# Kernel tuning notes

Hardware: AMD Instinct MI355X
Metric: run time of the kernel (lower is better)

## Reference

```python
import jax, jax.numpy as jnp
import numpy as np

B, C, H, W, D = 2, 512, 16, 16, 16
GROUPS = 32
EPS = 1e-6


def setup_inputs() -> dict:
    key = jax.random.key(0)
    ks = jax.random.split(key, 6)
    s = 1.0 / np.sqrt(C)
    inp = {
        "x": jax.random.normal(ks[0], (B, C, H, W, D), jnp.float32),
        "gn_w": jnp.ones((C,), jnp.float32),
        "gn_b": jnp.zeros((C,), jnp.float32),
        "wq": jax.random.normal(ks[1], (C, C), jnp.float32) * s,
        "bq": jnp.zeros((C,), jnp.float32),
        "wk": jax.random.normal(ks[2], (C, C), jnp.float32) * s,
        "bk": jnp.zeros((C,), jnp.float32),
        "wv": jax.random.normal(ks[3], (C, C), jnp.float32) * s,
        "bv": jnp.zeros((C,), jnp.float32),
        "wp": jax.random.normal(ks[4], (C, C), jnp.float32) * s,
        "bp": jnp.zeros((C,), jnp.float32),
    }
    return inp


def reference(x, gn_w, gn_b, wq, bq, wk, bk, wv, bv, wp, bp):
    b, c, h, w, d = x.shape
    # GroupNorm(32 groups, eps=1e-6, affine)
    xg = x.reshape(b, GROUPS, c // GROUPS, h, w, d)
    mu = xg.mean(axis=(2, 3, 4, 5), keepdims=True)
    var = xg.var(axis=(2, 3, 4, 5), keepdims=True)
    hn = ((xg - mu) / jnp.sqrt(var + EPS)).reshape(b, c, h, w, d)
    hn = hn * gn_w[None, :, None, None, None] + gn_b[None, :, None, None, None]
    # 1x1x1 conv projections == per-token channel matmul
    n = h * w * d
    hf = hn.reshape(b, c, n)
    q = jnp.einsum('oc,bcn->bon', wq, hf) + bq[None, :, None]  # [b,c,n]
    k = jnp.einsum('oc,bcn->bon', wk, hf) + bk[None, :, None]
    v = jnp.einsum('oc,bcn->bon', wv, hf) + bv[None, :, None]
    # attention: scores[b,i,j] = sum_c q[b,c,i] k[b,c,j] / sqrt(c)
    scores = jnp.einsum('bci,bcj->bij', q, k) * (c ** -0.5)
    attn = jax.nn.softmax(scores, axis=2)  # [b,n,n]
    # out[b,c,i] = sum_j v[b,c,j] attn[b,i,j]
    o = jnp.einsum('bij,bcj->bci', attn, v)
    o = jnp.einsum('oc,bcn->bon', wp, o) + bp[None, :, None]
    return x + o.reshape(b, c, h, w, d)
```

## Files before the change

### kernel.cpp

```cpp
#include <hip/hip_runtime.h>
#include <hip/hip_bf16.h>
#include <stdint.h>

typedef short short8 __attribute__((ext_vector_type(8)));
typedef float f32x4  __attribute__((ext_vector_type(4)));
typedef float f32x2  __attribute__((ext_vector_type(2)));
typedef float f32x16 __attribute__((ext_vector_type(16)));
typedef int   i32x4  __attribute__((ext_vector_type(4)));
typedef int   i32x8  __attribute__((ext_vector_type(8)));
typedef unsigned char uchar;

#define B_ 2
#define C_ 512
#define N_ 4096
#define G_ 32
#define WN (C_ * C_)
#define PREP_BLOCKS 4101

static __device__ __forceinline__ short f2bf(float f) {
    return __builtin_bit_cast(short, __float2bfloat16(f));
}
static __device__ __forceinline__ uchar f2fp8(float f) {
    return (uchar)(__builtin_amdgcn_cvt_pk_fp8_f32(f, f, 0, false) & 0xff);
}

static __device__ __forceinline__ void async16(uchar* lds_wave_base, const uchar* g) {
    auto l  = (__attribute__((address_space(3))) unsigned int*)(uintptr_t)(lds_wave_base);
    auto gg = (const __attribute__((address_space(1))) unsigned int*)(g);
    __builtin_amdgcn_global_load_lds(gg, l, 16, 0, 0);
}

__global__ void prep_stats(const float* __restrict__ wq, const float* __restrict__ wk,
                           const float* __restrict__ wv, const float* __restrict__ wp,
                           const float* __restrict__ bq, const float* __restrict__ bk,
                           const float* __restrict__ x,
                           uchar* __restrict__ Wb, float* __restrict__ bqk,
                           float* __restrict__ raw) {
    if (blockIdx.x < PREP_BLOCKS) {
        int i = blockIdx.x * 256 + threadIdx.x;
        if (i < 4 * WN) {
            const float* src = (i < 2*WN) ? ((i < WN) ? wq : wk) : ((i < 3*WN) ? wv : wp);
            Wb[i] = f2fp8(src[i & (WN - 1)] * 16.f);
        } else if (i < 4*WN + 1024) {
            int j = i - 4*WN;
            bqk[j] = (j < C_) ? bq[j] : bk[j - C_];
        }
        return;
    }
    const int idx = blockIdx.x - PREP_BLOCKS;
    const int bg = idx >> 2, qt = idx & 3;
    const float4* p = (const float4*)(x + (size_t)bg * 16 * N_ + (size_t)qt * 4 * N_);
    int tid = threadIdx.x;
    float s = 0.f, sq = 0.f;
    #pragma unroll
    for (int rep = 0; rep < 16; rep++) {
        float4 t = p[rep * 256 + tid];
        s  += t.x + t.y + t.z + t.w;
        sq += t.x*t.x + t.y*t.y + t.z*t.z + t.w*t.w;
    }
    __shared__ float rs[256], rq[256];
    rs[tid] = s; rq[tid] = sq;
    __syncthreads();
    for (int h = 128; h > 0; h >>= 1) {
        if (tid < h) { rs[tid] += rs[tid+h]; rq[tid] += rq[tid+h]; }
        __syncthreads();
    }
    if (tid == 0) {
        raw[idx*2+0] = rs[0];
        raw[idx*2+1] = rq[0];
    }
}

__global__ void gn_apply(const float* __restrict__ x, const float* __restrict__ raw,
                         const float* __restrict__ gw, const float* __restrict__ gb,
                         uchar* __restrict__ hn) {
    __shared__ uchar t[64 * 68];
    const int n0 = blockIdx.x * 64, c0 = blockIdx.y * 64, b = blockIdx.z;
    const int lane = threadIdx.x & 63, w = threadIdx.x >> 6;
    const float inv = 1.f / (16.f * N_);
    #pragma unroll
    for (int rep = 0; rep < 16; rep++) {
        int c  = rep * 4 + w;
        int cc = c0 + c;
        int g  = cc >> 4;
        int base = (b*G_ + g) * 8;
        float mean = (raw[base] + raw[base+2] + raw[base+4] + raw[base+6]) * inv;
        float var  = (raw[base+1] + raw[base+3] + raw[base+5] + raw[base+7]) * inv - mean * mean;
        float rstd = rsqrtf(var + 1e-6f);
        float sc = gw[cc] * rstd;
        float bi = gb[cc] - mean * sc;
        float v = x[((size_t)(b*C_ + cc)) * N_ + n0 + lane];
        t[lane*68 + c] = f2fp8(v * sc + bi);
    }
    __syncthreads();
    #pragma unroll
    for (int rep = 0; rep < 16; rep++) {
        int n = rep * 4 + w;
        hn[((size_t)(b*N_ + n0 + n)) * C_ + c0 + lane] = t[n*68 + lane];
    }
}

template<int BM, int BIAS_MODE, int OUT_MODE, int K, int SWZ>
__global__ __launch_bounds__(256, 3)
void gemm_nt8(const uchar* __restrict__ A, int lda, long long sAz,
              const uchar* __restrict__ Bm, int ldb, long long sBz,
              void* __restrict__ Cv, int ldc, long long sCz,
              const float* __restrict__ bias,
              const float* __restrict__ res,
              float alpha) {
    constexpr int MI = BM / 64;
    constexpr int T  = K / 64;
    constexpr int D  = (BM == 128) ? 4 : 3;
    constexpr unsigned WAITD = 0xF70u | D;
    constexpr unsigned WAIT0 = 0xF70u;
    __shared__ uchar As[3][BM * 64];
    __shared__ uchar Bs[3][128 * 64];

    int bx, by, bz;
    if (SWZ == 1) {
        int fid = blockIdx.x;
        int xcd = fid & 7, j = fid >> 3;
        int gg = (j >> 2) * 8 + xcd;
        bx = j & 3; by = gg & 63; bz = gg >> 6;
    } else if (SWZ == 2) {
        int fid = blockIdx.x;
        int xcd = fid & 7, j = fid >> 3;
        bz = j >> 7;
        int r = j & 127;
        by = (xcd << 2) | (r >> 5);
        bx = r & 31;
    } else { bx = blockIdx.x; by = blockIdx.y; bz = blockIdx.z; }

    const int tid  = threadIdx.x;
    const int lane = tid & 63;
    const int wid  = tid >> 6;
    const int wr   = wid >> 1;
    const int wc   = wid & 1;
    const int m0 = by * BM;
    const int n0 = bx * 128;

    const int r  = tid >> 2;
    const int gc = (tid & 3) ^ ((r >> 1) & 3);
    const uchar* Ap  = A  + sAz * bz + (size_t)(m0 + r) * lda + gc * 16;
    const uchar* Ap1 = Ap + (size_t)64 * lda;
    const uchar* Bp  = Bm + sBz * bz + (size_t)(n0 + r) * ldb + gc * 16;
    const uchar* Bp1 = Bp + (size_t)64 * ldb;

    f32x16 acc[MI][2];
    #pragma unroll
    for (int i = 0; i < MI; i++)
        #pragma unroll
        for (int j = 0; j < 2; j++)
            #pragma unroll
            for (int e = 0; e < 16; e++)
                acc[i][j][e] = 0.f;

    const int rl = lane & 31;
    const int hk = (lane >> 5) * 2;

    #define ISSUE(IB, u) do { size_t _kb = (size_t)(u) * 64; \
        async16(&As[IB][wid * 1024], Ap + _kb); \
        if (BM == 128) async16(&As[IB][4096 + wid * 1024], Ap1 + _kb); \
        async16(&Bs[IB][wid * 1024], Bp + _kb); \
        async16(&Bs[IB][4096 + wid * 1024], Bp1 + _kb); } while (0)

    #define STEP(Bf, DO_ISSUE, IB, u, DO_BAR, WIMM) do { \
        i32x8 af[MI], bf[2]; \
        _Pragma("unroll") \
        for (int i = 0; i < MI; i++) { \
            int ar = wr*(BM/2) + i*32 + rl; \
            int ao = ar*64 + ((hk ^ ((ar>>1)&3)) << 4); \
            *(i32x4*)&af[i]       = *(const i32x4*)&As[Bf][ao]; \
            *(((i32x4*)&af[i])+1) = *(const i32x4*)&As[Bf][ao ^ 16]; \
        } \
        _Pragma("unroll") \
        for (int i = 0; i < 2; i++) { \
            int br = wc*64 + i*32 + rl; \
            int bo = br*64 + ((hk ^ ((br>>1)&3)) << 4); \
            *(i32x4*)&bf[i]       = *(const i32x4*)&Bs[Bf][bo]; \
            *(((i32x4*)&bf[i])+1) = *(const i32x4*)&Bs[Bf][bo ^ 16]; \
        } \
        if (DO_ISSUE) ISSUE(IB, u); \
        _Pragma("unroll") \
        for (int mi = 0; mi < MI; mi++) \
            _Pragma("unroll") \
            for (int ni = 0; ni < 2; ni++) \
                acc[mi][ni] = __builtin_amdgcn_mfma_scale_f32_32x32x64_f8f6f4( \
                    af[mi], bf[ni], acc[mi][ni], 0, 0, 0, 127, 0, 127); \
        if (DO_BAR) { __builtin_amdgcn_s_waitcnt(WIMM); __builtin_amdgcn_s_barrier(); } \
    } while (0)

    ISSUE(0, 0);
    ISSUE(1, 1);
    __builtin_amdgcn_s_waitcnt(WAITD);
    __builtin_amdgcn_s_barrier();

    constexpr int Gm = (T - 2) / 3;
    for (int m = 0; m < Gm; m++) {
        STEP(0, 1, 2, m*3 + 2, 1, WAITD);
        STEP(1, 1, 0, m*3 + 3, 1, WAITD);
        STEP(2, 1, 1, m*3 + 4, 1, WAITD);
    }
    if (T - 3*Gm == 2) {
        STEP(0, 0, 0, 0, 1, WAIT0);
        STEP(1, 0, 0, 0, 0, 0);
    } else {
        STEP(0, 1, 2, T-2, 1, WAITD);
        STEP(1, 1, 0, T-1, 1, WAITD);
        STEP(2, 0, 0, 0, 1, WAIT0);
        STEP(0, 0, 0, 0, 0, 0);
    }
    #undef ISSUE
    #undef STEP

    const int rh = (lane >> 5) * 4;
    #pragma unroll
    for (int mi = 0; mi < MI; mi++) {
        #pragma unroll
        for (int ni = 0; ni < 2; ni++) {
            int cc = n0 + wc*64 + ni*32 + rl;
            float cb = (BIAS_MODE == 1) ? bias[cc] : 0.f;
            #pragma unroll
            for (int g = 0; g < 4; g++) {
                #pragma unroll
                for (int r4 = 0; r4 < 4; r4++) {
                    int rr = m0 + wr*(BM/2) + mi*32 + g*8 + rh + r4;
                    float val = acc[mi][ni][g*4 + r4] * alpha + cb;
                    if (BIAS_MODE == 2) val += bias[rr];
                    long long idx = sCz * bz + (long long)rr * ldc + cc;
                    if (OUT_MODE == 0)      ((short*)Cv)[idx] = f2bf(val);
                    else if (OUT_MODE == 2) ((float*)Cv)[idx] = val + res[idx];
                    else                    ((uchar*)Cv)[idx] = f2fp8(val);
                }
            }
        }
    }
}

__global__ void softmax_rows8(uchar* __restrict__ S) {
    const int lane = threadIdx.x & 63;
    const int wave = threadIdx.x >> 6;
    const size_t row = (size_t)blockIdx.x * 4 + wave;
    uint4* rp = (uint4*)(S + row * N_);
    uint4 d[4];
    float f[64];
    float mx = -3.0e38f;
    #pragma unroll
    for (int c = 0; c < 4; c++) {
        d[c] = rp[c * 64 + lane];
        unsigned wv[4] = {d[c].x, d[c].y, d[c].z, d[c].w};
        #pragma unroll
        for (int u = 0; u < 4; u++) {
            f32x2 lo = __builtin_amdgcn_cvt_pk_f32_fp8(wv[u], false);
            f32x2 hi = __builtin_amdgcn_cvt_pk_f32_fp8(wv[u], true);
            int b = c*16 + u*4;
            f[b+0] = lo[0]; f[b+1] = lo[1]; f[b+2] = hi[0]; f[b+3] = hi[1];
            mx = fmaxf(mx, fmaxf(fmaxf(lo[0], lo[1]), fmaxf(hi[0], hi[1])));
        }
    }
    #pragma unroll
    for (int off = 32; off > 0; off >>= 1)
        mx = fmaxf(mx, __shfl_xor(mx, off));
    float sum = 0.f;
    const float k = 0.0625f;
    #pragma unroll
    for (int j = 0; j < 64; j++) { f[j] = __expf((f[j] - mx) * k); sum += f[j]; }
    #pragma unroll
    for (int off = 32; off > 0; off >>= 1)
        sum += __shfl_xor(sum, off);
    float inv = 256.f / sum;
    #pragma unroll
    for (int c = 0; c < 4; c++) {
        unsigned wv[4];
        #pragma unroll
        for (int u = 0; u < 4; u++) {
            int b = c*16 + u*4;
            int o = 0;
            o = __builtin_amdgcn_cvt_pk_fp8_f32(f[b+0]*inv, f[b+1]*inv, o, false);
            o = __builtin_amdgcn_cvt_pk_fp8_f32(f[b+2]*inv, f[b+3]*inv, o, true);
            wv[u] = (unsigned)o;
        }
        uint4 ov; ov.x = wv[0]; ov.y = wv[1]; ov.z = wv[2]; ov.w = wv[3];
        rp[c * 64 + lane] = ov;
    }
}

extern "C" void kernel_launch(void* const* d_in, const int* in_sizes, int n_in,
                              void* d_out, int out_size, void* d_ws, size_t ws_size,
                              hipStream_t stream) {
    const float* x   = (const float*)d_in[0];
    const float* gnw = (const float*)d_in[1];
    const float* gnb = (const float*)d_in[2];
    const float* wq  = (const float*)d_in[3];
    const float* bq  = (const float*)d_in[4];
    const float* wk  = (const float*)d_in[5];
    const float* bk  = (const float*)d_in[6];
    const float* wv  = (const float*)d_in[7];
    const float* bv  = (const float*)d_in[8];
    const float* wp  = (const float*)d_in[9];
    const float* bp  = (const float*)d_in[10];
    float* out = (float*)d_out;
    char*  ws  = (char*)d_ws;

    float* raw = (float*)(ws + 0);
    float* bqk = (float*)(ws + 8192);
    uchar* Wb  = (uchar*)(ws + 65536);
    uchar* Hn  = (uchar*)(ws + (2ull  << 20));
    uchar* QK8 = (uchar*)(ws + (8ull  << 20));
    uchar* V8  = (uchar*)(ws + (16ull << 20));
    uchar* Ot8 = (uchar*)(ws + (20ull << 20));
    uchar* Sb  = (uchar*)(ws + (24ull << 20));

    prep_stats<<<PREP_BLOCKS + 256, 256, 0, stream>>>(wq, wk, wv, wp, bq, bk, x, Wb, bqk, raw);
    gn_apply<<<dim3(N_/64, C_/64, B_), 256, 0, stream>>>(x, raw, gnw, gnb, Hn);

    const long long sHn = (long long)N_ * C_;
    const long long sQK = (long long)N_ * 1024;
    const long long sV  = (long long)C_ * N_;
    const long long sS  = (long long)N_ * N_;

    gemm_nt8<128,1,3,512,0><<<dim3(8, 32, 2), 256, 0, stream>>>(
        Hn, C_, sHn, Wb, C_, 0, QK8, 1024, sQK, bqk, nullptr, 1.f/16.f);
    gemm_nt8<64,2,3,512,0><<<dim3(32, 8, 2), 256, 0, stream>>>(
        Wb + 2*WN, C_, 0, Hn, C_, sHn, V8, N_, sV, bv, nullptr, 1.f/16.f);

    const float alphaS = 0.044194173824159216f * 16.f;
    gemm_nt8<128,0,3,512,2><<<2048, 256, 0, stream>>>(
        QK8, 1024, sQK, QK8 + 512, 1024, sQK, Sb, N_, sS, nullptr, nullptr, alphaS);
    softmax_rows8<<<B_*N_/4, 256, 0, stream>>>(Sb);
    gemm_nt8<64,0,3,4096,1><<<512, 256, 0, stream>>>(
        Sb, N_, sS, V8, N_, sV, Ot8, C_, sHn, nullptr, nullptr, 1.f/16.f);
    gemm_nt8<64,2,2,512,0><<<dim3(32, 8, 2), 256, 0, stream>>>(
        Wb + 3*WN, C_, 0, Ot8, C_, sHn, out, N_, (long long)C_*N_, bp, x, 1.f/256.f);
}
```

Before: 188.0 us.

## Replace LDS-staged triple-buffered GEMM with direct global-to-register fragment loads

The fp8 GEMM kernel no longer stages A and B tiles through triple-buffered LDS with async global_load_lds and barriers. Each wave now loads its MFMA fragments straight from global memory into registers, unrolled four k-steps at a time, and the launch-bounds occupancy hint drops from 3 to 2 blocks to make room for the larger register footprint. This removes LDS traffic and barrier synchronisation. In exchange, waves in the same block no longer share tile loads, so global and L2 traffic goes up, and the loop has no software overlap between loads and MFMAs beyond what the unrolling gives.

```diff
diff --git a/kernel.cpp b/kernel.cpp
--- a/kernel.cpp
+++ b/kernel.cpp
@@ -22,12 +22,6 @@
 }
 static __device__ __forceinline__ uchar f2fp8(float f) {
     return (uchar)(__builtin_amdgcn_cvt_pk_fp8_f32(f, f, 0, false) & 0xff);
-}
-
-static __device__ __forceinline__ void async16(uchar* lds_wave_base, const uchar* g) {
-    auto l  = (__attribute__((address_space(3))) unsigned int*)(uintptr_t)(lds_wave_base);
-    auto gg = (const __attribute__((address_space(1))) unsigned int*)(g);
-    __builtin_amdgcn_global_load_lds(gg, l, 16, 0, 0);
 }
 
 __global__ void prep_stats(const float* __restrict__ wq, const float* __restrict__ wk,
@@ -101,7 +95,7 @@
 }
 
 template<int BM, int BIAS_MODE, int OUT_MODE, int K, int SWZ>
-__global__ __launch_bounds__(256, 3)
+__global__ __launch_bounds__(256, 2)
 void gemm_nt8(const uchar* __restrict__ A, int lda, long long sAz,
               const uchar* __restrict__ Bm, int ldb, long long sBz,
               void* __restrict__ Cv, int ldc, long long sCz,
@@ -110,11 +104,6 @@
               float alpha) {
     constexpr int MI = BM / 64;
     constexpr int T  = K / 64;
-    constexpr int D  = (BM == 128) ? 4 : 3;
-    constexpr unsigned WAITD = 0xF70u | D;
-    constexpr unsigned WAIT0 = 0xF70u;
-    __shared__ uchar As[3][BM * 64];
-    __shared__ uchar Bs[3][128 * 64];
 
     int bx, by, bz;
     if (SWZ == 1) {
@@ -139,12 +128,17 @@
     const int m0 = by * BM;
     const int n0 = bx * 128;
 
-    const int r  = tid >> 2;
-    const int gc = (tid & 3) ^ ((r >> 1) & 3);
-    const uchar* Ap  = A  + sAz * bz + (size_t)(m0 + r) * lda + gc * 16;
-    const uchar* Ap1 = Ap + (size_t)64 * lda;
-    const uchar* Bp  = Bm + sBz * bz + (size_t)(n0 + r) * ldb + gc * 16;
-    const uchar* Bp1 = Bp + (size_t)64 * ldb;
+    const int rl = lane & 31;
+    const int kh = (lane >> 5) * 32;
+
+    const uchar* Ab[MI];
+    #pragma unroll
+    for (int i = 0; i < MI; i++)
+        Ab[i] = A + sAz * bz + (size_t)(m0 + wr*(BM/2) + i*32 + rl) * lda + kh;
+    const uchar* Bb[2];
+    #pragma unroll
+    for (int i = 0; i < 2; i++)
+        Bb[i] = Bm + sBz * bz + (size_t)(n0 + wc*64 + i*32 + rl) * ldb + kh;
 
     f32x16 acc[MI][2];
     #pragma unroll
@@ -155,63 +149,35 @@
             for (int e = 0; e < 16; e++)
                 acc[i][j][e] = 0.f;
 
-    const int rl = lane & 31;
-    const int hk = (lane >> 5) * 2;
-
-    #define ISSUE(IB, u) do { size_t _kb = (size_t)(u) * 64; \
-        async16(&As[IB][wid * 1024], Ap + _kb); \
-        if (BM == 128) async16(&As[IB][4096 + wid * 1024], Ap1 + _kb); \
-        async16(&Bs[IB][wid * 1024], Bp + _kb); \
-        async16(&Bs[IB][4096 + wid * 1024], Bp1 + _kb); } while (0)
-
-    #define STEP(Bf, DO_ISSUE, IB, u, DO_BAR, WIMM) do { \
-        i32x8 af[MI], bf[2]; \
-        _Pragma("unroll") \
-        for (int i = 0; i < MI; i++) { \
-            int ar = wr*(BM/2) + i*32 + rl; \
-            int ao = ar*64 + ((hk ^ ((ar>>1)&3)) << 4); \
-            *(i32x4*)&af[i]       = *(const i32x4*)&As[Bf][ao]; \
-            *(((i32x4*)&af[i])+1) = *(const i32x4*)&As[Bf][ao ^ 16]; \
-        } \
-        _Pragma("unroll") \
-        for (int i = 0; i < 2; i++) { \
-            int br = wc*64 + i*32 + rl; \
-            int bo = br*64 + ((hk ^ ((br>>1)&3)) << 4); \
-            *(i32x4*)&bf[i]       = *(const i32x4*)&Bs[Bf][bo]; \
-            *(((i32x4*)&bf[i])+1) = *(const i32x4*)&Bs[Bf][bo ^ 16]; \
-        } \
-        if (DO_ISSUE) ISSUE(IB, u); \
-        _Pragma("unroll") \
-        for (int mi = 0; mi < MI; mi++) \
-            _Pragma("unroll") \
-            for (int ni = 0; ni < 2; ni++) \
-                acc[mi][ni] = __builtin_amdgcn_mfma_scale_f32_32x32x64_f8f6f4( \
-                    af[mi], bf[ni], acc[mi][ni], 0, 0, 0, 127, 0, 127); \
-        if (DO_BAR) { __builtin_amdgcn_s_waitcnt(WIMM); __builtin_amdgcn_s_barrier(); } \
-    } while (0)
-
-    ISSUE(0, 0);
-    ISSUE(1, 1);
-    __builtin_amdgcn_s_waitcnt(WAITD);
-    __builtin_amdgcn_s_barrier();
-
-    constexpr int Gm = (T - 2) / 3;
-    for (int m = 0; m < Gm; m++) {
-        STEP(0, 1, 2, m*3 + 2, 1, WAITD);
-        STEP(1, 1, 0, m*3 + 3, 1, WAITD);
-        STEP(2, 1, 1, m*3 + 4, 1, WAITD);
-    }
-    if (T - 3*Gm == 2) {
-        STEP(0, 0, 0, 0, 1, WAIT0);
-        STEP(1, 0, 0, 0, 0, 0);
-    } else {
-        STEP(0, 1, 2, T-2, 1, WAITD);
-        STEP(1, 1, 0, T-1, 1, WAITD);
-        STEP(2, 0, 0, 0, 1, WAIT0);
-        STEP(0, 0, 0, 0, 0, 0);
-    }
-    #undef ISSUE
-    #undef STEP
+    for (int uo = 0; uo < T / 4; uo++) {
+        i32x8 af[4][MI], bf[4][2];
+        #pragma unroll
+        for (int ui = 0; ui < 4; ui++) {
+            int kb = ui * 64;
+            #pragma unroll
+            for (int i = 0; i < MI; i++) {
+                *(i32x4*)&af[ui][i]       = *(const i32x4*)(Ab[i] + kb);
+                *(((i32x4*)&af[ui][i])+1) = *(const i32x4*)(Ab[i] + kb + 16);
+            }
+            #pragma unroll
+            for (int i = 0; i < 2; i++) {
+                *(i32x4*)&bf[ui][i]       = *(const i32x4*)(Bb[i] + kb);
+                *(((i32x4*)&bf[ui][i])+1) = *(const i32x4*)(Bb[i] + kb + 16);
+            }
+        }
+        #pragma unroll
+        for (int ui = 0; ui < 4; ui++)
+            #pragma unroll
+            for (int mi = 0; mi < MI; mi++)
+                #pragma unroll
+                for (int ni = 0; ni < 2; ni++)
+                    acc[mi][ni] = __builtin_amdgcn_mfma_scale_f32_32x32x64_f8f6f4(
+                        af[ui][mi], bf[ui][ni], acc[mi][ni], 0, 0, 0, 127, 0, 127);
+        #pragma unroll
+        for (int i = 0; i < MI; i++) Ab[i] += 256;
+        #pragma unroll
+        for (int i = 0; i < 2; i++)  Bb[i] += 256;
+    }
 
     const int rh = (lane >> 5) * 4;
     #pragma unroll
```

Result: slower. 310.8 us (+65.4%).
